# Kernel tuning notes

Measured on AMD Instinct MI355X. Metric: run time of the kernel, lower is better.

Reference implementation:

```python
import jax, jax.numpy as jnp
import numpy as np
from jax import lax

V, E, H, B, T = 50000, 100, 64, 128, 1024


def setup_inputs() -> dict:
    key = jax.random.key(0)
    ks = jax.random.split(key, 16)
    def u(k, shape, fan):
        s = 1.0 / np.sqrt(fan)
        return jax.random.uniform(k, shape, jnp.float32, -s, s)
    x = jax.random.randint(ks[0], (B, T), 0, V)
    emb = jax.random.normal(ks[1], (V, E), jnp.float32)
    emb = emb.at[0].set(0.0)  # padding_idx=0
    return {
        'x': x,
        'emb': emb,
        'Wih0': u(ks[2], (4 * H, E), H), 'Whh0': u(ks[3], (4 * H, H), H),
        'bih0': u(ks[4], (4 * H,), H), 'bhh0': u(ks[5], (4 * H,), H),
        'Wih1': u(ks[6], (4 * H, H), H), 'Whh1': u(ks[7], (4 * H, H), H),
        'bih1': u(ks[8], (4 * H,), H), 'bhh1': u(ks[9], (4 * H,), H),
        'W1': u(ks[10], (H, H), H), 'b1': u(ks[11], (H,), H),
        'W2': u(ks[12], (1, H), H), 'b2': u(ks[13], (1,), H),
    }


def lstm_layer(inp, Wih, Whh, bih, bhh):
    # inp: [B, T, D]; PyTorch gate order i, f, g, o
    b, h = inp.shape[0], Whh.shape[1]
    xw = jnp.einsum('btd,gd->btg', inp, Wih) + bih + bhh  # [B, T, 4H]
    def step(carry, xw_t):
        hs, cs = carry
        gates = xw_t + hs @ Whh.T
        i, f, g, o = jnp.split(gates, 4, axis=-1)
        cs = jax.nn.sigmoid(f) * cs + jax.nn.sigmoid(i) * jnp.tanh(g)
        hs = jax.nn.sigmoid(o) * jnp.tanh(cs)
        return (hs, cs), hs
    init = (jnp.zeros((b, h), inp.dtype), jnp.zeros((b, h), inp.dtype))
    _, out = lax.scan(step, init, jnp.swapaxes(xw, 0, 1))  # [T, B, H]
    return jnp.swapaxes(out, 0, 1)


def reference(x, emb, Wih0, Whh0, bih0, bhh0, Wih1, Whh1, bih1, bhh1, W1, b1, W2, b2):
    e = emb[x]                                  # [B, T, E]
    h0 = lstm_layer(e, Wih0, Whh0, bih0, bhh0)  # [B, T, H]
    h1 = lstm_layer(h0, Wih1, Whh1, bih1, bhh1) # [B, T, H]
    last = h1[:, -1, :]                         # [B, H]
    z = jax.nn.relu(last @ W1.T + b1)           # dropout is identity in eval
    return jax.nn.sigmoid(z @ W2.T + b2)        # [B, 1]
```

## Files before the change

kernel.cpp:

```cpp
#include <hip/hip_runtime.h>
#include <hip/hip_bf16.h>

#define EMB_D 100
#define HID 64
#define G4 256
#define BATCH 128
#define SEQ 1024
#define TOK 64

typedef _Float16 half2v __attribute__((ext_vector_type(2)));
typedef unsigned short u16;
typedef unsigned int   u32;

__device__ __forceinline__ float rcpf(float x) { return __builtin_amdgcn_rcpf(x); }
__device__ __forceinline__ float sigf(float x) { return rcpf(1.0f + __expf(-x)); }
__device__ __forceinline__ float tanh_fast(float x) {
  float t = __expf(-2.0f * fabsf(x));
  float r = (1.0f - t) * rcpf(1.0f + t);
  return copysignf(r, x);
}
__device__ __forceinline__ float dot2(u32 h, u32 w, float acc) {
  return __builtin_amdgcn_fdot2(__builtin_bit_cast(half2v, h),
                                __builtin_bit_cast(half2v, w), acc, false);
}
__device__ __forceinline__ u32 packh2(float lo, float hi) {
  u16 a = __builtin_bit_cast(u16, (_Float16)lo);
  u16 b = __builtin_bit_cast(u16, (_Float16)hi);
  return (u32)a | ((u32)b << 16);
}
#define QP_XOR1 0xB1
#define QP_XOR2 0x4E
#define QP_XOR3 0x1B
#define QPERM(x, ctrl)                                                        \
  __builtin_bit_cast(float, __builtin_amdgcn_mov_dpp(                         \
      __builtin_bit_cast(int, (x)), (ctrl), 0xF, 0xF, true))

__global__ void prep_kernel(const float* __restrict__ Wih0,
                            const float* __restrict__ Whh0, const float* __restrict__ Wih1,
                            const float* __restrict__ Whh1,
                            const float* __restrict__ bih0, const float* __restrict__ bhh0,
                            const float* __restrict__ bih1, const float* __restrict__ bhh1,
                            u32* __restrict__ Wih0T2, float* __restrict__ b0c,
                            float* __restrict__ b1c,
                            u32* __restrict__ Whh0h, u32* __restrict__ Wih1h,
                            u32* __restrict__ Whh1h) {
  int g = threadIdx.x;
  b0c[g] = bih0[g] + bhh0[g];
  b1c[g] = bih1[g] + bhh1[g];
  for (int dp = 0; dp < 50; ++dp)
    Wih0T2[dp * G4 + g] = packh2(Wih0[g * EMB_D + 2 * dp], Wih0[g * EMB_D + 2 * dp + 1]);
  for (int d = 0; d < 32; ++d) {
    Whh0h[g * 32 + d] = packh2(Whh0[g * HID + 2 * d], Whh0[g * HID + 2 * d + 1]);
    Wih1h[g * 32 + d] = packh2(Wih1[g * HID + 2 * d], Wih1[g * HID + 2 * d + 1]);
    Whh1h[g * 32 + d] = packh2(Whh1[g * HID + 2 * d], Whh1[g * HID + 2 * d + 1]);
  }
}

__global__ __attribute__((amdgpu_waves_per_eu(1, 4))) __launch_bounds__(256)
void xw0_kernel(
    const int* __restrict__ x, const float* __restrict__ emb,
    const u32* __restrict__ Wih0T2, const float* __restrict__ b0c,
    _Float16* __restrict__ xw0h) {
  __shared__ int sidx[TOK];
  __shared__ alignas(16) u32 erow[TOK][52];
  int g = threadIdx.x;
  long t0 = (long)blockIdx.x * TOK;

  if (g < TOK) sidx[g] = x[t0 + g];
  __syncthreads();
  for (int i = g; i < TOK * 50; i += 256) {
    int tok = i / 50, dp = i - tok * 50;
    const float* er = emb + (size_t)sidx[tok] * EMB_D + 2 * dp;
    erow[tok][dp] = packh2(er[0], er[1]);
  }
  for (int i = g; i < TOK * 2; i += 256) erow[i >> 1][50 + (i & 1)] = 0;

  u32 wreg[52];
  #pragma unroll
  for (int dp = 0; dp < 50; ++dp) wreg[dp] = Wih0T2[dp * G4 + g];
  wreg[50] = 0; wreg[51] = 0;
  float bb = b0c[g];
  __syncthreads();

  for (int tok = 0; tok < TOK; ++tok) {
    const uint4* ep = (const uint4*)erow[tok];
    float a0 = bb, a1 = 0.f, a2 = 0.f, a3 = 0.f;
    #pragma unroll
    for (int c = 0; c < 13; ++c) {
      uint4 hv = ep[c];
      a0 = dot2(hv.x, wreg[4 * c],     a0);
      a1 = dot2(hv.y, wreg[4 * c + 1], a1);
      a2 = dot2(hv.z, wreg[4 * c + 2], a2);
      a3 = dot2(hv.w, wreg[4 * c + 3], a3);
    }
    xw0h[(t0 + tok) * G4 + g] = (_Float16)((a0 + a1) + (a2 + a3));
  }
}

__global__ __launch_bounds__(512, 2) void lstm_fused_kernel(
    const _Float16* __restrict__ xw0h,
    const u32* __restrict__ Whh0h, const u32* __restrict__ Wih1h,
    const u32* __restrict__ Whh1h, const float* __restrict__ b1c,
    const float* __restrict__ W1, const float* __restrict__ clsb1,
    const float* __restrict__ W2, const float* __restrict__ clsb2,
    float* __restrict__ out) {
  int tid = threadIdx.x;
  int lane = tid & 63;
  int w = tid >> 6;
  bool isL1 = (w >= 4);
  int eg = isL1 ? (w - 4) : w;
  int e = eg * 16 + (lane >> 2);
  int k = lane & 3;
  int row = k * HID + e;
  int b = blockIdx.x;

  __shared__ alignas(16) _Float16 h0s[3][HID];
  __shared__ alignas(16) _Float16 h1s[2][HID];
  __shared__ float ps[2][4][65];
  __shared__ alignas(16) float hf[HID];

  uint4 wA[8], wP[4];
  if (!isL1) {
    const uint4* p = (const uint4*)(Whh0h + row * 32);
    #pragma unroll
    for (int c = 0; c < 8; ++c) wA[c] = p[c];
    const uint4* q = (const uint4*)(Wih1h + row * 32);
    #pragma unroll
    for (int c = 0; c < 4; ++c) wP[c] = q[c];
  } else {
    const uint4* q = (const uint4*)(Wih1h + row * 32);
    #pragma unroll
    for (int c = 0; c < 4; ++c) wP[c] = q[4 + c];
    const uint4* p = (const uint4*)(Whh1h + row * 32);
    #pragma unroll
    for (int c = 0; c < 8; ++c) wA[c] = p[c];
  }
  float bias = isL1 ? b1c[row] : 0.f;

  if (tid < 3 * HID) ((u16*)h0s)[tid] = 0;
  if (tid < 2 * HID) ((u16*)h1s)[tid] = 0;

  const _Float16* xr = xw0h + (long)b * SEQ * G4 + row;
  float xw_t = 0.f, xw_t1 = 0.f;
  if (!isL1) { xw_t = (float)xr[0]; xw_t1 = (float)xr[G4]; }
  float c_reg = 0.f;
  __syncthreads();

  int h0w = 0, h0rA = 2, h0rB = 1;
  for (int t = 0; t <= SEQ + 1; ++t) {
    if (!isL1) {
      if (t <= SEQ) {
        const uint4* h0p = (const uint4*)h0s[h0rA];
        uint4 hc[8];
        #pragma unroll
        for (int c = 0; c < 8; ++c) hc[c] = h0p[c];
        {
          float p0 = 0.f, p1 = 0.f, p2 = 0.f, p3 = 0.f;
          #pragma unroll
          for (int c = 0; c < 4; ++c) {
            p0 = dot2(hc[c].x, wP[c].x, p0);
            p1 = dot2(hc[c].y, wP[c].y, p1);
            p2 = dot2(hc[c].z, wP[c].z, p2);
            p3 = dot2(hc[c].w, wP[c].w, p3);
          }
          ps[t & 1][k][e] = (p0 + p1) + (p2 + p3);
        }
        if (t < SEQ) {
          float a0 = xw_t, a1 = 0.f, a2 = 0.f, a3 = 0.f;
          #pragma unroll
          for (int c = 0; c < 8; ++c) {
            a0 = dot2(hc[c].x, wA[c].x, a0);
            a1 = dot2(hc[c].y, wA[c].y, a1);
            a2 = dot2(hc[c].z, wA[c].z, a2);
            a3 = dot2(hc[c].w, wA[c].w, a3);
          }
          float gown = (a0 + a1) + (a2 + a3);
          float gx1 = QPERM(gown, QP_XOR1);
          float gx2 = QPERM(gown, QP_XOR2);
          float gx3 = QPERM(gown, QP_XOR3);
          c_reg = sigf(gx1) * c_reg + sigf(gown) * tanh_fast(gx2);
          float hv = sigf(gx3) * tanh_fast(c_reg);
          if (k == 0) h0s[h0w][e] = (_Float16)hv;
          float xw_t2 = 0.f;
          int tn = (t + 2 < SEQ) ? (t + 2) : (SEQ - 1);
          xw_t2 = (float)xr[(long)tn * G4];
          xw_t = xw_t1; xw_t1 = xw_t2;
        }
      }
    } else {
      if (t >= 2) {
        const uint4* h0p = (const uint4*)h0s[h0rB];
        const uint4* h1p = (const uint4*)h1s[(t + 1) & 1];
        float a0 = bias, a1 = 0.f, a2 = 0.f, a3 = 0.f;
        float b0 = 0.f, b1 = 0.f, b2 = 0.f, b3 = 0.f;
        #pragma unroll
        for (int c = 0; c < 4; ++c) {
          uint4 h = h0p[4 + c];
          a0 = dot2(h.x, wP[c].x, a0);
          a1 = dot2(h.y, wP[c].y, a1);
          a2 = dot2(h.z, wP[c].z, a2);
          a3 = dot2(h.w, wP[c].w, a3);
        }
        #pragma unroll
        for (int c = 0; c < 8; ++c) {
          uint4 h = h1p[c];
          b0 = dot2(h.x, wA[c].x, b0);
          b1 = dot2(h.y, wA[c].y, b1);
          b2 = dot2(h.z, wA[c].z, b2);
          b3 = dot2(h.w, wA[c].w, b3);
        }
        float gown = ((a0 + a1) + (a2 + a3)) + ((b0 + b1) + (b2 + b3))
                     + ps[(t + 1) & 1][k][e];
        float gx1 = QPERM(gown, QP_XOR1);
        float gx2 = QPERM(gown, QP_XOR2);
        float gx3 = QPERM(gown, QP_XOR3);
        c_reg = sigf(gx1) * c_reg + sigf(gown) * tanh_fast(gx2);
        float hv = sigf(gx3) * tanh_fast(c_reg);
        if (k == 0) {
          h1s[t & 1][e] = (_Float16)hv;
          if (t == SEQ + 1) hf[e] = hv;
        }
      }
    }
    h0w = (h0w == 2) ? 0 : h0w + 1;
    h0rA = (h0rA == 2) ? 0 : h0rA + 1;
    h0rB = (h0rB == 2) ? 0 : h0rB + 1;
    asm volatile("s_waitcnt lgkmcnt(0)" ::: "memory");
    __builtin_amdgcn_s_barrier();
    asm volatile("" ::: "memory");
  }

  if (w == 0) {
    int j = lane;
    const float4* wp = (const float4*)(W1 + j * HID);
    const float4* hp = (const float4*)hf;
    float z0 = clsb1[j], z1 = 0.f, z2 = 0.f, z3 = 0.f;
    #pragma unroll
    for (int c = 0; c < 16; ++c) {
      float4 wv = wp[c];
      float4 hv = hp[c];
      z0 = fmaf(hv.x, wv.x, z0);
      z1 = fmaf(hv.y, wv.y, z1);
      z2 = fmaf(hv.z, wv.z, z2);
      z3 = fmaf(hv.w, wv.w, z3);
    }
    float z = fmaxf((z0 + z1) + (z2 + z3), 0.f);
    float v = z * W2[j];
    v += __shfl_xor(v, 1);
    v += __shfl_xor(v, 2);
    v += __shfl_xor(v, 4);
    v += __shfl_xor(v, 8);
    v += __shfl_xor(v, 16);
    v += __shfl_xor(v, 32);
    if (lane == 0) out[b] = sigf(v + clsb2[0]);
  }
}

extern "C" void kernel_launch(void* const* d_in, const int* in_sizes, int n_in,
                              void* d_out, int out_size, void* d_ws, size_t ws_size,
                              hipStream_t stream) {
  const int*   x    = (const int*)d_in[0];
  const float* emb  = (const float*)d_in[1];
  const float* Wih0 = (const float*)d_in[2];
  const float* Whh0 = (const float*)d_in[3];
  const float* bih0 = (const float*)d_in[4];
  const float* bhh0 = (const float*)d_in[5];
  const float* Wih1 = (const float*)d_in[6];
  const float* Whh1 = (const float*)d_in[7];
  const float* bih1 = (const float*)d_in[8];
  const float* bhh1 = (const float*)d_in[9];
  const float* W1   = (const float*)d_in[10];
  const float* b1   = (const float*)d_in[11];
  const float* W2   = (const float*)d_in[12];
  const float* b2   = (const float*)d_in[13];
  float* out = (float*)d_out;

  char* ws = (char*)d_ws;
  const size_t XW0_BYTES = (size_t)BATCH * SEQ * G4 * sizeof(_Float16);
  _Float16* xw0h = (_Float16*)ws;     ws += XW0_BYTES;
  u32* Wih0T2    = (u32*)ws;          ws += (size_t)50 * G4 * sizeof(u32);
  float* b0c     = (float*)ws;        ws += G4 * sizeof(float);
  float* b1c     = (float*)ws;        ws += G4 * sizeof(float);
  u32* Whh0h     = (u32*)ws;          ws += (size_t)G4 * 32 * sizeof(u32);
  u32* Wih1h     = (u32*)ws;          ws += (size_t)G4 * 32 * sizeof(u32);
  u32* Whh1h     = (u32*)ws;          ws += (size_t)G4 * 32 * sizeof(u32);

  prep_kernel<<<1, 256, 0, stream>>>(Wih0, Whh0, Wih1, Whh1, bih0, bhh0, bih1, bhh1,
                                     Wih0T2, b0c, b1c, Whh0h, Wih1h, Whh1h);
  xw0_kernel<<<(BATCH * SEQ) / TOK, 256, 0, stream>>>(x, emb, Wih0T2, b0c, xw0h);
  lstm_fused_kernel<<<BATCH, 512, 0, stream>>>(xw0h, Whh0h, Wih1h, Whh1h, b1c,
                                               W1, b1, W2, b2, out);
}
```

Baseline: 782.8 us.

## Run both LSTM layers in the same waves and pre-scale weights by log2e

```diff
diff --git a/kernel.cpp b/kernel.cpp
--- a/kernel.cpp
+++ b/kernel.cpp
@@ -7,18 +7,25 @@
 #define BATCH 128
 #define SEQ 1024
 #define TOK 64
+#define LOG2E 1.44269504f
 
 typedef _Float16 half2v __attribute__((ext_vector_type(2)));
 typedef unsigned short u16;
 typedef unsigned int   u32;
 
 __device__ __forceinline__ float rcpf(float x) { return __builtin_amdgcn_rcpf(x); }
-__device__ __forceinline__ float sigf(float x) { return rcpf(1.0f + __expf(-x)); }
-__device__ __forceinline__ float tanh_fast(float x) {
-  float t = __expf(-2.0f * fabsf(x));
-  float r = (1.0f - t) * rcpf(1.0f + t);
-  return copysignf(r, x);
-}
+__device__ __forceinline__ float ex2(float x) { return __builtin_amdgcn_exp2f(x); }
+__device__ __forceinline__ float sig_pre(float xp) { return rcpf(1.0f + ex2(-xp)); }
+__device__ __forceinline__ float tanh_pre(float xp) {
+  float t = ex2(-2.0f * fabsf(xp));
+  return copysignf((1.0f - t) * rcpf(1.0f + t), xp);
+}
+__device__ __forceinline__ float tanh_nat(float x) {
+  float t = ex2(-2.885390082f * fabsf(x));
+  return copysignf((1.0f - t) * rcpf(1.0f + t), x);
+}
+__device__ __forceinline__ float sig_nat(float x) { return rcpf(1.0f + ex2(-LOG2E * x)); }
+
 __device__ __forceinline__ float dot2(u32 h, u32 w, float acc) {
   return __builtin_amdgcn_fdot2(__builtin_bit_cast(half2v, h),
                                 __builtin_bit_cast(half2v, w), acc, false);
@@ -45,14 +52,15 @@
                             u32* __restrict__ Whh0h, u32* __restrict__ Wih1h,
                             u32* __restrict__ Whh1h) {
   int g = threadIdx.x;
-  b0c[g] = bih0[g] + bhh0[g];
-  b1c[g] = bih1[g] + bhh1[g];
+  b0c[g] = (bih0[g] + bhh0[g]) * LOG2E;
+  b1c[g] = (bih1[g] + bhh1[g]) * LOG2E;
   for (int dp = 0; dp < 50; ++dp)
-    Wih0T2[dp * G4 + g] = packh2(Wih0[g * EMB_D + 2 * dp], Wih0[g * EMB_D + 2 * dp + 1]);
+    Wih0T2[dp * G4 + g] = packh2(Wih0[g * EMB_D + 2 * dp] * LOG2E,
+                                 Wih0[g * EMB_D + 2 * dp + 1] * LOG2E);
   for (int d = 0; d < 32; ++d) {
-    Whh0h[g * 32 + d] = packh2(Whh0[g * HID + 2 * d], Whh0[g * HID + 2 * d + 1]);
-    Wih1h[g * 32 + d] = packh2(Wih1[g * HID + 2 * d], Wih1[g * HID + 2 * d + 1]);
-    Whh1h[g * 32 + d] = packh2(Whh1[g * HID + 2 * d], Whh1[g * HID + 2 * d + 1]);
+    Whh0h[g * 32 + d] = packh2(Whh0[g * HID + 2 * d] * LOG2E, Whh0[g * HID + 2 * d + 1] * LOG2E);
+    Wih1h[g * 32 + d] = packh2(Wih1[g * HID + 2 * d] * LOG2E, Wih1[g * HID + 2 * d + 1] * LOG2E);
+    Whh1h[g * 32 + d] = packh2(Whh1[g * HID + 2 * d] * LOG2E, Whh1[g * HID + 2 * d + 1] * LOG2E);
   }
 }
 
@@ -97,7 +105,8 @@
   }
 }
 
-__global__ __launch_bounds__(512, 2) void lstm_fused_kernel(
+__global__ __attribute__((amdgpu_waves_per_eu(1, 1))) __launch_bounds__(256)
+void lstm_fused_kernel(
     const _Float16* __restrict__ xw0h,
     const u32* __restrict__ Whh0h, const u32* __restrict__ Wih1h,
     const u32* __restrict__ Whh1h, const float* __restrict__ b1c,
@@ -105,133 +114,107 @@
     const float* __restrict__ W2, const float* __restrict__ clsb2,
     float* __restrict__ out) {
   int tid = threadIdx.x;
-  int lane = tid & 63;
+  int l = tid & 63;
   int w = tid >> 6;
-  bool isL1 = (w >= 4);
-  int eg = isL1 ? (w - 4) : w;
-  int e = eg * 16 + (lane >> 2);
-  int k = lane & 3;
+  int e = w * 16 + (l >> 2);
+  int k = l & 3;
   int row = k * HID + e;
   int b = blockIdx.x;
 
-  __shared__ alignas(16) _Float16 h0s[3][HID];
+  __shared__ alignas(16) _Float16 h0s[2][HID];
   __shared__ alignas(16) _Float16 h1s[2][HID];
-  __shared__ float ps[2][4][65];
   __shared__ alignas(16) float hf[HID];
 
-  uint4 wA[8], wP[4];
-  if (!isL1) {
-    const uint4* p = (const uint4*)(Whh0h + row * 32);
+  uint4 w0[8], w1[8], w2[8];
+  {
+    const uint4* p0 = (const uint4*)(Whh0h + row * 32);
+    const uint4* p1 = (const uint4*)(Wih1h + row * 32);
+    const uint4* p2 = (const uint4*)(Whh1h + row * 32);
     #pragma unroll
-    for (int c = 0; c < 8; ++c) wA[c] = p[c];
-    const uint4* q = (const uint4*)(Wih1h + row * 32);
-    #pragma unroll
-    for (int c = 0; c < 4; ++c) wP[c] = q[c];
-  } else {
-    const uint4* q = (const uint4*)(Wih1h + row * 32);
-    #pragma unroll
-    for (int c = 0; c < 4; ++c) wP[c] = q[4 + c];
-    const uint4* p = (const uint4*)(Whh1h + row * 32);
-    #pragma unroll
-    for (int c = 0; c < 8; ++c) wA[c] = p[c];
-  }
-  float bias = isL1 ? b1c[row] : 0.f;
-
-  if (tid < 3 * HID) ((u16*)h0s)[tid] = 0;
-  if (tid < 2 * HID) ((u16*)h1s)[tid] = 0;
+    for (int c = 0; c < 8; ++c) { w0[c] = p0[c]; w1[c] = p1[c]; w2[c] = p2[c]; }
+  }
+  #pragma unroll
+  for (int c = 0; c < 8; ++c) {
+    asm volatile("" : "+v"(w0[c].x), "+v"(w0[c].y), "+v"(w0[c].z), "+v"(w0[c].w));
+    asm volatile("" : "+v"(w1[c].x), "+v"(w1[c].y), "+v"(w1[c].z), "+v"(w1[c].w));
+    asm volatile("" : "+v"(w2[c].x), "+v"(w2[c].y), "+v"(w2[c].z), "+v"(w2[c].w));
+  }
+  float bias = b1c[row];
+
+  if (tid < 128) ((u16*)h0s)[tid] = 0;
+  else           ((u16*)h1s)[tid - 128] = 0;
 
   const _Float16* xr = xw0h + (long)b * SEQ * G4 + row;
-  float xw_t = 0.f, xw_t1 = 0.f;
-  if (!isL1) { xw_t = (float)xr[0]; xw_t1 = (float)xr[G4]; }
-  float c_reg = 0.f;
-  __syncthreads();
-
-  int h0w = 0, h0rA = 2, h0rB = 1;
-  for (int t = 0; t <= SEQ + 1; ++t) {
-    if (!isL1) {
-      if (t <= SEQ) {
-        const uint4* h0p = (const uint4*)h0s[h0rA];
-        uint4 hc[8];
-        #pragma unroll
-        for (int c = 0; c < 8; ++c) hc[c] = h0p[c];
-        {
-          float p0 = 0.f, p1 = 0.f, p2 = 0.f, p3 = 0.f;
-          #pragma unroll
-          for (int c = 0; c < 4; ++c) {
-            p0 = dot2(hc[c].x, wP[c].x, p0);
-            p1 = dot2(hc[c].y, wP[c].y, p1);
-            p2 = dot2(hc[c].z, wP[c].z, p2);
-            p3 = dot2(hc[c].w, wP[c].w, p3);
-          }
-          ps[t & 1][k][e] = (p0 + p1) + (p2 + p3);
-        }
-        if (t < SEQ) {
-          float a0 = xw_t, a1 = 0.f, a2 = 0.f, a3 = 0.f;
-          #pragma unroll
-          for (int c = 0; c < 8; ++c) {
-            a0 = dot2(hc[c].x, wA[c].x, a0);
-            a1 = dot2(hc[c].y, wA[c].y, a1);
-            a2 = dot2(hc[c].z, wA[c].z, a2);
-            a3 = dot2(hc[c].w, wA[c].w, a3);
-          }
-          float gown = (a0 + a1) + (a2 + a3);
-          float gx1 = QPERM(gown, QP_XOR1);
-          float gx2 = QPERM(gown, QP_XOR2);
-          float gx3 = QPERM(gown, QP_XOR3);
-          c_reg = sigf(gx1) * c_reg + sigf(gown) * tanh_fast(gx2);
-          float hv = sigf(gx3) * tanh_fast(c_reg);
-          if (k == 0) h0s[h0w][e] = (_Float16)hv;
-          float xw_t2 = 0.f;
-          int tn = (t + 2 < SEQ) ? (t + 2) : (SEQ - 1);
-          xw_t2 = (float)xr[(long)tn * G4];
-          xw_t = xw_t1; xw_t1 = xw_t2;
-        }
+  float xw_t = (float)xr[0];
+  float xw_t1 = (float)xr[G4];
+  float c0 = 0.f, c1 = 0.f;
+  __syncthreads();
+
+  for (int t = 0; t <= SEQ; ++t) {
+    int rb = (t + 1) & 1, wb = t & 1;
+    uint4 hc0[8], hc1[8];
+    {
+      const uint4* p0 = (const uint4*)h0s[rb];
+      const uint4* p1 = (const uint4*)h1s[rb];
+      #pragma unroll
+      for (int c = 0; c < 8; ++c) { hc0[c] = p0[c]; hc1[c] = p1[c]; }
+    }
+    int tn = (t + 2 < SEQ) ? (t + 2) : (SEQ - 1);
+    float xw_t2 = (float)xr[(long)tn * G4];
+
+    if (t < SEQ) {
+      float a0 = xw_t, a1 = 0.f, a2 = 0.f, a3 = 0.f;
+      #pragma unroll
+      for (int c = 0; c < 8; ++c) {
+        a0 = dot2(hc0[c].x, w0[c].x, a0);
+        a1 = dot2(hc0[c].y, w0[c].y, a1);
+        a2 = dot2(hc0[c].z, w0[c].z, a2);
+        a3 = dot2(hc0[c].w, w0[c].w, a3);
       }
-    } else {
-      if (t >= 2) {
-        const uint4* h0p = (const uint4*)h0s[h0rB];
-        const uint4* h1p = (const uint4*)h1s[(t + 1) & 1];
-        float a0 = bias, a1 = 0.f, a2 = 0.f, a3 = 0.f;
-        float b0 = 0.f, b1 = 0.f, b2 = 0.f, b3 = 0.f;
-        #pragma unroll
-        for (int c = 0; c < 4; ++c) {
-          uint4 h = h0p[4 + c];
-          a0 = dot2(h.x, wP[c].x, a0);
-          a1 = dot2(h.y, wP[c].y, a1);
-          a2 = dot2(h.z, wP[c].z, a2);
-          a3 = dot2(h.w, wP[c].w, a3);
-        }
-        #pragma unroll
-        for (int c = 0; c < 8; ++c) {
-          uint4 h = h1p[c];
-          b0 = dot2(h.x, wA[c].x, b0);
-          b1 = dot2(h.y, wA[c].y, b1);
-          b2 = dot2(h.z, wA[c].z, b2);
-          b3 = dot2(h.w, wA[c].w, b3);
-        }
-        float gown = ((a0 + a1) + (a2 + a3)) + ((b0 + b1) + (b2 + b3))
-                     + ps[(t + 1) & 1][k][e];
-        float gx1 = QPERM(gown, QP_XOR1);
-        float gx2 = QPERM(gown, QP_XOR2);
-        float gx3 = QPERM(gown, QP_XOR3);
-        c_reg = sigf(gx1) * c_reg + sigf(gown) * tanh_fast(gx2);
-        float hv = sigf(gx3) * tanh_fast(c_reg);
-        if (k == 0) {
-          h1s[t & 1][e] = (_Float16)hv;
-          if (t == SEQ + 1) hf[e] = hv;
-        }
+      float g0 = (a0 + a1) + (a2 + a3);
+      float g0x1 = QPERM(g0, QP_XOR1);
+      float g0x2 = QPERM(g0, QP_XOR2);
+      float g0x3 = QPERM(g0, QP_XOR3);
+      c0 = sig_pre(g0x1) * c0 + sig_pre(g0) * tanh_pre(g0x2);
+      float hv0 = sig_pre(g0x3) * tanh_nat(c0);
+      if (k == 0) h0s[wb][e] = (_Float16)hv0;
+    }
+
+    if (t >= 1) {
+      float a0 = bias, a1 = 0.f, a2 = 0.f, a3 = 0.f;
+      float b0 = 0.f, b1 = 0.f, b2 = 0.f, b3 = 0.f;
+      #pragma unroll
+      for (int c = 0; c < 8; ++c) {
+        a0 = dot2(hc0[c].x, w1[c].x, a0);
+        a1 = dot2(hc0[c].y, w1[c].y, a1);
+        a2 = dot2(hc0[c].z, w1[c].z, a2);
+        a3 = dot2(hc0[c].w, w1[c].w, a3);
+        b0 = dot2(hc1[c].x, w2[c].x, b0);
+        b1 = dot2(hc1[c].y, w2[c].y, b1);
+        b2 = dot2(hc1[c].z, w2[c].z, b2);
+        b3 = dot2(hc1[c].w, w2[c].w, b3);
       }
-    }
-    h0w = (h0w == 2) ? 0 : h0w + 1;
-    h0rA = (h0rA == 2) ? 0 : h0rA + 1;
-    h0rB = (h0rB == 2) ? 0 : h0rB + 1;
+      float g1 = ((a0 + a1) + (a2 + a3)) + ((b0 + b1) + (b2 + b3));
+      float g1x1 = QPERM(g1, QP_XOR1);
+      float g1x2 = QPERM(g1, QP_XOR2);
+      float g1x3 = QPERM(g1, QP_XOR3);
+      c1 = sig_pre(g1x1) * c1 + sig_pre(g1) * tanh_pre(g1x2);
+      float hv1 = sig_pre(g1x3) * tanh_nat(c1);
+      if (k == 0) {
+        h1s[wb][e] = (_Float16)hv1;
+        if (t == SEQ) hf[e] = hv1;
+      }
+    }
+
+    xw_t = xw_t1; xw_t1 = xw_t2;
     asm volatile("s_waitcnt lgkmcnt(0)" ::: "memory");
     __builtin_amdgcn_s_barrier();
     asm volatile("" ::: "memory");
   }
+  __syncthreads();
 
   if (w == 0) {
-    int j = lane;
+    int j = l;
     const float4* wp = (const float4*)(W1 + j * HID);
     const float4* hp = (const float4*)hf;
     float z0 = clsb1[j], z1 = 0.f, z2 = 0.f, z3 = 0.f;
@@ -252,7 +235,7 @@
     v += __shfl_xor(v, 8);
     v += __shfl_xor(v, 16);
     v += __shfl_xor(v, 32);
-    if (lane == 0) out[b] = sigf(v + clsb2[0]);
+    if (l == 0) out[b] = sig_nat(v + clsb2[0]);
   }
 }
 
@@ -288,6 +271,6 @@
   prep_kernel<<<1, 256, 0, stream>>>(Wih0, Whh0, Wih1, Whh1, bih0, bhh0, bih1, bhh1,
                                      Wih0T2, b0c, b1c, Whh0h, Wih1h, Whh1h);
   xw0_kernel<<<(BATCH * SEQ) / TOK, 256, 0, stream>>>(x, emb, Wih0T2, b0c, xw0h);
-  lstm_fused_kernel<<<BATCH, 512, 0, stream>>>(xw0h, Whh0h, Wih1h, Whh1h, b1c,
+  lstm_fused_kernel<<<BATCH, 256, 0, stream>>>(xw0h, Whh0h, Wih1h, Whh1h, b1c,
                                                W1, b1, W2, b2, out);
 }
```

Result: faster. 737.6 us (-5.8%).

## Prescale LSTM weights by log2e and use exp2; restructure layer-1 LDS loads

Applied to the files above, without the earlier changes.

```diff
diff --git a/kernel.cpp b/kernel.cpp
--- a/kernel.cpp
+++ b/kernel.cpp
@@ -7,18 +7,25 @@
 #define BATCH 128
 #define SEQ 1024
 #define TOK 64
+#define LOG2E 1.44269504f
 
 typedef _Float16 half2v __attribute__((ext_vector_type(2)));
 typedef unsigned short u16;
 typedef unsigned int   u32;
 
 __device__ __forceinline__ float rcpf(float x) { return __builtin_amdgcn_rcpf(x); }
-__device__ __forceinline__ float sigf(float x) { return rcpf(1.0f + __expf(-x)); }
-__device__ __forceinline__ float tanh_fast(float x) {
-  float t = __expf(-2.0f * fabsf(x));
-  float r = (1.0f - t) * rcpf(1.0f + t);
-  return copysignf(r, x);
-}
+__device__ __forceinline__ float ex2(float x) { return __builtin_amdgcn_exp2f(x); }
+__device__ __forceinline__ float sig_pre(float xp) { return rcpf(1.0f + ex2(-xp)); }
+__device__ __forceinline__ float tanh_pre(float xp) {
+  float t = ex2(-2.0f * fabsf(xp));
+  return copysignf((1.0f - t) * rcpf(1.0f + t), xp);
+}
+__device__ __forceinline__ float tanh_nat(float x) {
+  float t = ex2(-2.885390082f * fabsf(x));
+  return copysignf((1.0f - t) * rcpf(1.0f + t), x);
+}
+__device__ __forceinline__ float sig_nat(float x) { return rcpf(1.0f + ex2(-LOG2E * x)); }
+
 __device__ __forceinline__ float dot2(u32 h, u32 w, float acc) {
   return __builtin_amdgcn_fdot2(__builtin_bit_cast(half2v, h),
                                 __builtin_bit_cast(half2v, w), acc, false);
@@ -45,14 +52,15 @@
                             u32* __restrict__ Whh0h, u32* __restrict__ Wih1h,
                             u32* __restrict__ Whh1h) {
   int g = threadIdx.x;
-  b0c[g] = bih0[g] + bhh0[g];
-  b1c[g] = bih1[g] + bhh1[g];
+  b0c[g] = (bih0[g] + bhh0[g]) * LOG2E;
+  b1c[g] = (bih1[g] + bhh1[g]) * LOG2E;
   for (int dp = 0; dp < 50; ++dp)
-    Wih0T2[dp * G4 + g] = packh2(Wih0[g * EMB_D + 2 * dp], Wih0[g * EMB_D + 2 * dp + 1]);
+    Wih0T2[dp * G4 + g] = packh2(Wih0[g * EMB_D + 2 * dp] * LOG2E,
+                                 Wih0[g * EMB_D + 2 * dp + 1] * LOG2E);
   for (int d = 0; d < 32; ++d) {
-    Whh0h[g * 32 + d] = packh2(Whh0[g * HID + 2 * d], Whh0[g * HID + 2 * d + 1]);
-    Wih1h[g * 32 + d] = packh2(Wih1[g * HID + 2 * d], Wih1[g * HID + 2 * d + 1]);
-    Whh1h[g * 32 + d] = packh2(Whh1[g * HID + 2 * d], Whh1[g * HID + 2 * d + 1]);
+    Whh0h[g * 32 + d] = packh2(Whh0[g * HID + 2 * d] * LOG2E, Whh0[g * HID + 2 * d + 1] * LOG2E);
+    Wih1h[g * 32 + d] = packh2(Wih1[g * HID + 2 * d] * LOG2E, Wih1[g * HID + 2 * d + 1] * LOG2E);
+    Whh1h[g * 32 + d] = packh2(Whh1[g * HID + 2 * d] * LOG2E, Whh1[g * HID + 2 * d + 1] * LOG2E);
   }
 }
 
@@ -97,7 +105,8 @@
   }
 }
 
-__global__ __launch_bounds__(512, 2) void lstm_fused_kernel(
+__global__ __attribute__((amdgpu_waves_per_eu(1, 2))) __launch_bounds__(512)
+void lstm_fused_kernel(
     const _Float16* __restrict__ xw0h,
     const u32* __restrict__ Whh0h, const u32* __restrict__ Wih1h,
     const u32* __restrict__ Whh1h, const float* __restrict__ b1c,
@@ -105,22 +114,21 @@
     const float* __restrict__ W2, const float* __restrict__ clsb2,
     float* __restrict__ out) {
   int tid = threadIdx.x;
-  int lane = tid & 63;
+  int l = tid & 63;
   int w = tid >> 6;
-  bool isL1 = (w >= 4);
-  int eg = isL1 ? (w - 4) : w;
-  int e = eg * 16 + (lane >> 2);
-  int k = lane & 3;
+  bool lo = (w < 4);
+  int e = (w & 3) * 16 + (l >> 2);
+  int k = l & 3;
   int row = k * HID + e;
   int b = blockIdx.x;
 
   __shared__ alignas(16) _Float16 h0s[3][HID];
   __shared__ alignas(16) _Float16 h1s[2][HID];
-  __shared__ float ps[2][4][65];
+  __shared__ float ps[2][HID][4];
   __shared__ alignas(16) float hf[HID];
 
   uint4 wA[8], wP[4];
-  if (!isL1) {
+  if (lo) {
     const uint4* p = (const uint4*)(Whh0h + row * 32);
     #pragma unroll
     for (int c = 0; c < 8; ++c) wA[c] = p[c];
@@ -135,35 +143,45 @@
     #pragma unroll
     for (int c = 0; c < 8; ++c) wA[c] = p[c];
   }
-  float bias = isL1 ? b1c[row] : 0.f;
+  #pragma unroll
+  for (int c = 0; c < 8; ++c)
+    asm volatile("" : "+v"(wA[c].x), "+v"(wA[c].y), "+v"(wA[c].z), "+v"(wA[c].w));
+  #pragma unroll
+  for (int c = 0; c < 4; ++c)
+    asm volatile("" : "+v"(wP[c].x), "+v"(wP[c].y), "+v"(wP[c].z), "+v"(wP[c].w));
+
+  float bias = lo ? 0.f : b1c[row];
 
   if (tid < 3 * HID) ((u16*)h0s)[tid] = 0;
-  if (tid < 2 * HID) ((u16*)h1s)[tid] = 0;
+  else if (tid < 5 * HID) ((u16*)h1s)[tid - 3 * HID] = 0;
 
   const _Float16* xr = xw0h + (long)b * SEQ * G4 + row;
   float xw_t = 0.f, xw_t1 = 0.f;
-  if (!isL1) { xw_t = (float)xr[0]; xw_t1 = (float)xr[G4]; }
+  if (lo) { xw_t = (float)xr[0]; xw_t1 = (float)xr[G4]; }
   float c_reg = 0.f;
   __syncthreads();
 
-  int h0w = 0, h0rA = 2, h0rB = 1;
+  int rbLo = 2, rbHi = 1, wbH0 = 0;
   for (int t = 0; t <= SEQ + 1; ++t) {
-    if (!isL1) {
+    if (lo) {
       if (t <= SEQ) {
-        const uint4* h0p = (const uint4*)h0s[h0rA];
         uint4 hc[8];
-        #pragma unroll
-        for (int c = 0; c < 8; ++c) hc[c] = h0p[c];
+        const uint4* hp = (const uint4*)h0s[rbLo];
+        #pragma unroll
+        for (int c = 0; c < 8; ++c) hc[c] = hp[c];
         {
-          float p0 = 0.f, p1 = 0.f, p2 = 0.f, p3 = 0.f;
+          float p0 = dot2(hc[0].x, wP[0].x, 0.f);
+          float p1 = dot2(hc[0].y, wP[0].y, 0.f);
+          float p2 = dot2(hc[0].z, wP[0].z, 0.f);
+          float p3 = dot2(hc[0].w, wP[0].w, 0.f);
           #pragma unroll
-          for (int c = 0; c < 4; ++c) {
+          for (int c = 1; c < 4; ++c) {
             p0 = dot2(hc[c].x, wP[c].x, p0);
             p1 = dot2(hc[c].y, wP[c].y, p1);
             p2 = dot2(hc[c].z, wP[c].z, p2);
             p3 = dot2(hc[c].w, wP[c].w, p3);
           }
-          ps[t & 1][k][e] = (p0 + p1) + (p2 + p3);
+          ps[t & 1][e][k] = (p0 + p1) + (p2 + p3);
         }
         if (t < SEQ) {
           float a0 = xw_t, a1 = 0.f, a2 = 0.f, a3 = 0.f;
@@ -174,64 +192,70 @@
             a2 = dot2(hc[c].z, wA[c].z, a2);
             a3 = dot2(hc[c].w, wA[c].w, a3);
           }
-          float gown = (a0 + a1) + (a2 + a3);
-          float gx1 = QPERM(gown, QP_XOR1);
-          float gx2 = QPERM(gown, QP_XOR2);
-          float gx3 = QPERM(gown, QP_XOR3);
-          c_reg = sigf(gx1) * c_reg + sigf(gown) * tanh_fast(gx2);
-          float hv = sigf(gx3) * tanh_fast(c_reg);
-          if (k == 0) h0s[h0w][e] = (_Float16)hv;
-          float xw_t2 = 0.f;
+          float g0 = (a0 + a1) + (a2 + a3);
+          float gx1 = QPERM(g0, QP_XOR1);
+          float gx2 = QPERM(g0, QP_XOR2);
+          float gx3 = QPERM(g0, QP_XOR3);
+          c_reg = sig_pre(gx1) * c_reg + sig_pre(g0) * tanh_pre(gx2);
+          float hv = sig_pre(gx3) * tanh_nat(c_reg);
+          if (k == 0) h0s[wbH0][e] = (_Float16)hv;
           int tn = (t + 2 < SEQ) ? (t + 2) : (SEQ - 1);
-          xw_t2 = (float)xr[(long)tn * G4];
+          float xw_t2 = (float)xr[(long)tn * G4];
           xw_t = xw_t1; xw_t1 = xw_t2;
         }
       }
     } else {
       if (t >= 2) {
-        const uint4* h0p = (const uint4*)h0s[h0rB];
-        const uint4* h1p = (const uint4*)h1s[(t + 1) & 1];
+        const uint4* hp0 = (const uint4*)h0s[rbHi];
+        const uint4* hp1 = (const uint4*)h1s[(t + 1) & 1];
+        uint4 hh[4], h1c[8];
+        #pragma unroll
+        for (int c = 0; c < 4; ++c) hh[c] = hp0[4 + c];
+        #pragma unroll
+        for (int c = 0; c < 8; ++c) h1c[c] = hp1[c];
+        float psv = ps[(t + 1) & 1][e][k];
         float a0 = bias, a1 = 0.f, a2 = 0.f, a3 = 0.f;
-        float b0 = 0.f, b1 = 0.f, b2 = 0.f, b3 = 0.f;
         #pragma unroll
         for (int c = 0; c < 4; ++c) {
-          uint4 h = h0p[4 + c];
-          a0 = dot2(h.x, wP[c].x, a0);
-          a1 = dot2(h.y, wP[c].y, a1);
-          a2 = dot2(h.z, wP[c].z, a2);
-          a3 = dot2(h.w, wP[c].w, a3);
-        }
-        #pragma unroll
-        for (int c = 0; c < 8; ++c) {
-          uint4 h = h1p[c];
-          b0 = dot2(h.x, wA[c].x, b0);
-          b1 = dot2(h.y, wA[c].y, b1);
-          b2 = dot2(h.z, wA[c].z, b2);
-          b3 = dot2(h.w, wA[c].w, b3);
-        }
-        float gown = ((a0 + a1) + (a2 + a3)) + ((b0 + b1) + (b2 + b3))
-                     + ps[(t + 1) & 1][k][e];
-        float gx1 = QPERM(gown, QP_XOR1);
-        float gx2 = QPERM(gown, QP_XOR2);
-        float gx3 = QPERM(gown, QP_XOR3);
-        c_reg = sigf(gx1) * c_reg + sigf(gown) * tanh_fast(gx2);
-        float hv = sigf(gx3) * tanh_fast(c_reg);
+          a0 = dot2(hh[c].x, wP[c].x, a0);
+          a1 = dot2(hh[c].y, wP[c].y, a1);
+          a2 = dot2(hh[c].z, wP[c].z, a2);
+          a3 = dot2(hh[c].w, wP[c].w, a3);
+        }
+        float b0 = dot2(h1c[0].x, wA[0].x, 0.f);
+        float b1 = dot2(h1c[0].y, wA[0].y, 0.f);
+        float b2 = dot2(h1c[0].z, wA[0].z, 0.f);
+        float b3 = dot2(h1c[0].w, wA[0].w, 0.f);
+        #pragma unroll
+        for (int c = 1; c < 8; ++c) {
+          b0 = dot2(h1c[c].x, wA[c].x, b0);
+          b1 = dot2(h1c[c].y, wA[c].y, b1);
+          b2 = dot2(h1c[c].z, wA[c].z, b2);
+          b3 = dot2(h1c[c].w, wA[c].w, b3);
+        }
+        float g1 = (((a0 + a1) + (a2 + a3)) + ((b0 + b1) + (b2 + b3))) + psv;
+        float gx1 = QPERM(g1, QP_XOR1);
+        float gx2 = QPERM(g1, QP_XOR2);
+        float gx3 = QPERM(g1, QP_XOR3);
+        c_reg = sig_pre(gx1) * c_reg + sig_pre(g1) * tanh_pre(gx2);
+        float hv = sig_pre(gx3) * tanh_nat(c_reg);
         if (k == 0) {
           h1s[t & 1][e] = (_Float16)hv;
           if (t == SEQ + 1) hf[e] = hv;
         }
       }
     }
-    h0w = (h0w == 2) ? 0 : h0w + 1;
-    h0rA = (h0rA == 2) ? 0 : h0rA + 1;
-    h0rB = (h0rB == 2) ? 0 : h0rB + 1;
+    rbLo = (rbLo == 2) ? 0 : rbLo + 1;
+    rbHi = (rbHi == 2) ? 0 : rbHi + 1;
+    wbH0 = (wbH0 == 2) ? 0 : wbH0 + 1;
     asm volatile("s_waitcnt lgkmcnt(0)" ::: "memory");
     __builtin_amdgcn_s_barrier();
     asm volatile("" ::: "memory");
   }
+  __syncthreads();
 
   if (w == 0) {
-    int j = lane;
+    int j = l;
     const float4* wp = (const float4*)(W1 + j * HID);
     const float4* hp = (const float4*)hf;
     float z0 = clsb1[j], z1 = 0.f, z2 = 0.f, z3 = 0.f;
@@ -252,7 +276,7 @@
     v += __shfl_xor(v, 8);
     v += __shfl_xor(v, 16);
     v += __shfl_xor(v, 32);
-    if (lane == 0) out[b] = sigf(v + clsb2[0]);
+    if (l == 0) out[b] = sig_nat(v + clsb2[0]);
   }
 }
 
```

After: 768.9 us. About the same (-1.8%).
